# Optimization experiments

Measured on AMD Instinct MI355X. Metric: run time of the kernel, lower is better.

## Reference

```python
import jax, jax.numpy as jnp
import numpy as np

HID = 32
IN = 6
B, T = 512, 2048

def setup_inputs() -> dict:
    key = jax.random.key(0)
    ks = jax.random.split(key, 8)
    s = 1.0 / np.sqrt(HID)  # torch GRU/Linear default init scale
    return {
        "acc": jax.random.normal(ks[0], (B, T, 3), dtype=jnp.float32),
        "mag": jax.random.normal(ks[1], (B, T, 3), dtype=jnp.float32),
        "W_ih": jax.random.uniform(ks[2], (3 * HID, IN), dtype=jnp.float32, minval=-s, maxval=s),
        "W_hh": jax.random.uniform(ks[3], (3 * HID, HID), dtype=jnp.float32, minval=-s, maxval=s),
        "b_ih": jax.random.uniform(ks[4], (3 * HID,), dtype=jnp.float32, minval=-s, maxval=s),
        "b_hh": jax.random.uniform(ks[5], (3 * HID,), dtype=jnp.float32, minval=-s, maxval=s),
        "Wq": jax.random.uniform(ks[6], (4, HID), dtype=jnp.float32, minval=-s, maxval=s),
        "bq": jax.random.uniform(ks[7], (4,), dtype=jnp.float32, minval=-s, maxval=s),
    }

def _gru_seq(x, W_ih, W_hh, b_ih, b_hh):
    # x: [B,T,6] -> hidden states [B,T,HID]; PyTorch gate order: r, z, n
    gi = jnp.einsum('bti,gi->btg', x, W_ih) + b_ih  # [B,T,3H] precomputed input gates
    h0 = jnp.zeros((x.shape[0], HID), dtype=x.dtype)

    def step(h, gi_t):
        gh = h @ W_hh.T + b_hh                      # [B,3H]
        ir, iz, inn = jnp.split(gi_t, 3, axis=-1)
        hr, hz, hn = jnp.split(gh, 3, axis=-1)
        r = jax.nn.sigmoid(ir + hr)
        z = jax.nn.sigmoid(iz + hz)
        n = jnp.tanh(inn + r * hn)
        h_new = (1.0 - z) * n + z * h
        return h_new, h_new

    _, hs = jax.lax.scan(step, h0, jnp.swapaxes(gi, 0, 1))  # hs: [T,B,H]
    return jnp.swapaxes(hs, 0, 1)

def reference(acc, mag, W_ih, W_hh, b_ih, b_hh, Wq, bq):
    x = jnp.concatenate([acc, mag], axis=-1)        # [B,T,6]
    out = _gru_seq(x, W_ih, W_hh, b_ih, b_hh)       # [B,T,H]
    q = out @ Wq.T + bq                             # [B,T,4]
    return q / jnp.linalg.norm(q, axis=-1, keepdims=True)
```

## Files before the change

kernel.cpp:

```cpp
#include <hip/hip_runtime.h>
#include <hip/hip_bf16.h>

typedef float f2  __attribute__((ext_vector_type(2)));
typedef float f4v __attribute__((ext_vector_type(4)));

#ifndef __has_builtin
#define __has_builtin(x) 0
#endif

#define HID   32
#define TLEN  2048
#define BATCH 512
#define L2E   1.4426950408889634f

__device__ __forceinline__ float fast_rcp(float x) {
#if __has_builtin(__builtin_amdgcn_rcpf)
    return __builtin_amdgcn_rcpf(x);
#else
    return 1.0f / x;
#endif
}
__device__ __forceinline__ float fast_rsq(float x) {
#if __has_builtin(__builtin_amdgcn_rsqf)
    return __builtin_amdgcn_rsqf(x);
#else
    return rsqrtf(x);
#endif
}
__device__ __forceinline__ float fast_exp2(float x) {
#if __has_builtin(__builtin_amdgcn_exp2f)
    return __builtin_amdgcn_exp2f(x);
#else
    return exp2f(x);
#endif
}

__device__ __forceinline__ float xor32_sum(float x) {
#if __has_builtin(__builtin_amdgcn_permlane32_swap)
    typedef unsigned int u2v __attribute__((ext_vector_type(2)));
    u2v r = __builtin_amdgcn_permlane32_swap(__float_as_uint(x), __float_as_uint(x),
                                             false, false);
    return __uint_as_float(r.x) + __uint_as_float(r.y);
#else
    float a = x, b = x;
    asm("v_permlane32_swap_b32 %0, %1" : "+&v"(a), "+&v"(b));
    return a + b;
#endif
}

#if __has_builtin(__builtin_amdgcn_ds_swizzle)
#define SWZ_XOR(x, XORM) \
    __int_as_float(__builtin_amdgcn_ds_swizzle(__float_as_int(x), ((XORM) << 10) | 0x1F))
#else
#define SWZ_XOR(x, XORM) __shfl_xor((x), (XORM))
#endif

#define ELT(arr, i) ((i) % 4 == 0 ? (arr)[(i)/4].x : \
                     (i) % 4 == 1 ? (arr)[(i)/4].y : \
                     (i) % 4 == 2 ? (arr)[(i)/4].z : (arr)[(i)/4].w)

__global__ __launch_bounds__(64) void gru_fused_kernel(
    const float* __restrict__ acc_g, const float* __restrict__ mag_g,
    const float* __restrict__ W_ih, const float* __restrict__ W_hh,
    const float* __restrict__ b_ih, const float* __restrict__ b_hh,
    const float* __restrict__ Wq, const float* __restrict__ bq,
    float* __restrict__ out)
{
    const int lane = threadIdx.x;
    const int j    = lane & 31;
    const int half = lane >> 5;
    const int kb   = half * 16;
    const int b    = blockIdx.x;

    const int tq = lane >> 3;
    const int kq = (lane >> 2) & 1;
    const int m  = lane & 3;

    __shared__ float hbuf[8 * HID];

    f2 wr[8], wz[8], wn[8];
#pragma unroll
    for (int p = 0; p < 8; ++p) {
        wr[p] = L2E          * *reinterpret_cast<const f2*>(W_hh + (0 * HID + j) * HID + kb + 2 * p);
        wz[p] = L2E          * *reinterpret_cast<const f2*>(W_hh + (1 * HID + j) * HID + kb + 2 * p);
        wn[p] = (2.0f * L2E) * *reinterpret_cast<const f2*>(W_hh + (2 * HID + j) * HID + kb + 2 * p);
    }
    f4v wq4[4];
#pragma unroll
    for (int i = 0; i < 4; ++i)
        wq4[i] = *reinterpret_cast<const f4v*>(Wq + m * HID + kq * 16 + 4 * i);

    float wir[6], wiz[6], win[6];
#pragma unroll
    for (int i = 0; i < 6; ++i) {
        wir[i] = 0.5f * L2E * W_ih[(0 * HID + j) * 6 + i];
        wiz[i] = 0.5f * L2E * W_ih[(1 * HID + j) * 6 + i];
        win[i] = 2.0f * L2E * W_ih[(2 * HID + j) * 6 + i];
    }
    const float br_s  = 0.5f * L2E * (b_ih[0 * HID + j] + b_hh[0 * HID + j]);
    const float bz_s  = 0.5f * L2E * (b_ih[1 * HID + j] + b_hh[1 * HID + j]);
    const float bhn_s = L2E * b_hh[2 * HID + j];
    const float bin_s = 2.0f * L2E * b_ih[2 * HID + j];
    const float bqv   = bq[m];

    hbuf[7 * HID + j] = 0.0f;

    const float* accp = acc_g + (size_t)b * TLEN * 3;
    const float* magp = mag_g + (size_t)b * TLEN * 3;
    float* outp = out + (size_t)b * TLEN * 4;

    float h = 0.0f;

    auto step = [&](int sp, int ss, float a0, float a1, float a2,
                                    float m0, float m1, float m2) {
        const float* hb = &hbuf[sp * HID + kb];
        f4v A = *reinterpret_cast<const f4v*>(hb + 0);
        f4v B = *reinterpret_cast<const f4v*>(hb + 4);
        f4v C = *reinterpret_cast<const f4v*>(hb + 8);
        f4v D = *reinterpret_cast<const f4v*>(hb + 12);
        f2 hp[8] = { {A.x,A.y},{A.z,A.w},{B.x,B.y},{B.z,B.w},
                     {C.x,C.y},{C.z,C.w},{D.x,D.y},{D.z,D.w} };

        f2 dr0 = wr[0] * hp[0]; f2 dr1 = wr[4] * hp[4];
        f2 dz0 = wz[0] * hp[0]; f2 dz1 = wz[4] * hp[4];
        f2 dn0 = wn[0] * hp[0]; f2 dn1 = wn[4] * hp[4];
#pragma unroll
        for (int p = 1; p < 4; ++p) {
            dr0 += wr[p] * hp[p];  dr1 += wr[p + 4] * hp[p + 4];
            dz0 += wz[p] * hp[p];  dz1 += wz[p + 4] * hp[p + 4];
            dn0 += wn[p] * hp[p];  dn1 += wn[p + 4] * hp[p + 4];
        }

        float gr = fmaf(a2, wir[2], fmaf(a1, wir[1], fmaf(a0, wir[0], br_s)));
        gr = fmaf(m2, wir[5], fmaf(m1, wir[4], fmaf(m0, wir[3], gr)));
        float gz = fmaf(a2, wiz[2], fmaf(a1, wiz[1], fmaf(a0, wiz[0], bz_s)));
        gz = fmaf(m2, wiz[5], fmaf(m1, wiz[4], fmaf(m0, wiz[3], gz)));
        float gn = fmaf(a2, win[2], fmaf(a1, win[1], fmaf(a0, win[0], bin_s)));
        gn = fmaf(m2, win[5], fmaf(m1, win[4], fmaf(m0, win[3], gn)));

        f2 drs = dr0 + dr1; float sr = drs.x + drs.y + gr;
        f2 dzs = dz0 + dz1; float sz = dzs.x + dzs.y + gz;
        f2 dns = dn0 + dn1; float hn = dns.x + dns.y + bhn_s;
        sr = xor32_sum(sr);
        sz = xor32_sum(sz);
        hn = xor32_sum(hn);

        float r = fast_rcp(1.0f + fast_exp2(-sr));
        float z = fast_rcp(1.0f + fast_exp2(-sz));
        float ap = fmaf(r, hn, gn);
        ap = fmaxf(ap, -30.0f);
        float u  = fast_exp2(-ap);
        float nn = (1.0f - u) * fast_rcp(1.0f + u);
        h = fmaf(z, h - nn, nn);
        hbuf[ss * HID + j] = h;
    };

    auto qbatch = [&](int t0) {
        const float* hq = &hbuf[tq * HID + kq * 16];
        f4v QA = *reinterpret_cast<const f4v*>(hq + 0);
        f4v QB = *reinterpret_cast<const f4v*>(hq + 4);
        f4v QC = *reinterpret_cast<const f4v*>(hq + 8);
        f4v QD = *reinterpret_cast<const f4v*>(hq + 12);
        f4v qa = QA * wq4[0];
        qa += QB * wq4[1];
        qa += QC * wq4[2];
        qa += QD * wq4[3];
        float qp = (qa.x + qa.y) + (qa.z + qa.w);
        qp += SWZ_XOR(qp, 4);
        qp += bqv;
        float s = qp * qp;
        s += SWZ_XOR(s, 1);
        s += SWZ_XOR(s, 2);
        float qv = qp * fast_rsq(s);
        if (!(lane & 4))
            outp[(size_t)(t0 + tq) * 4 + m] = qv;
    };

    f4v xaA[6], xmA[6], xaB[6], xmB[6];
#pragma unroll
    for (int w = 0; w < 6; ++w) {
        xaA[w] = *reinterpret_cast<const f4v*>(accp + 4 * w);
        xmA[w] = *reinterpret_cast<const f4v*>(magp + 4 * w);
    }

#define WINDOW(XA, XM, XA_N, XM_N, T0)                                         \
    {                                                                          \
        const int tn = ((T0) + 8 < TLEN) ? ((T0) + 8) * 3 : 0;                 \
        _Pragma("unroll")                                                      \
        for (int w = 0; w < 6; ++w) {                                          \
            XA_N[w] = *reinterpret_cast<const f4v*>(accp + tn + 4 * w);        \
            XM_N[w] = *reinterpret_cast<const f4v*>(magp + tn + 4 * w);        \
        }                                                                      \
        _Pragma("unroll")                                                      \
        for (int s = 0; s < 8; ++s) {                                          \
            step((s + 7) & 7, s,                                               \
                 ELT(XA, 3 * s + 0), ELT(XA, 3 * s + 1), ELT(XA, 3 * s + 2),   \
                 ELT(XM, 3 * s + 0), ELT(XM, 3 * s + 1), ELT(XM, 3 * s + 2));  \
        }                                                                      \
        qbatch(T0);                                                            \
    }

    for (int t0 = 0; t0 < TLEN; t0 += 16) {
        WINDOW(xaA, xmA, xaB, xmB, t0);
        WINDOW(xaB, xmB, xaA, xmA, t0 + 8);
    }
#undef WINDOW
}

extern "C" void kernel_launch(void* const* d_in, const int* in_sizes, int n_in,
                              void* d_out, int out_size, void* d_ws, size_t ws_size,
                              hipStream_t stream) {
    const float* acc  = (const float*)d_in[0];
    const float* mag  = (const float*)d_in[1];
    const float* W_ih = (const float*)d_in[2];
    const float* W_hh = (const float*)d_in[3];
    const float* b_ih = (const float*)d_in[4];
    const float* b_hh = (const float*)d_in[5];
    const float* Wq   = (const float*)d_in[6];
    const float* bq   = (const float*)d_in[7];

    gru_fused_kernel<<<dim3(BATCH), dim3(64), 0, stream>>>(
        acc, mag, W_ih, W_hh, b_ih, b_hh, Wq, bq, (float*)d_out);
}
```

Measured before the change: 601.6 us.

## Stage input windows through shared memory with one scalar load per lane

```diff
diff --git a/kernel.cpp b/kernel.cpp
--- a/kernel.cpp
+++ b/kernel.cpp
@@ -11,6 +11,7 @@
 #define HID   32
 #define TLEN  2048
 #define BATCH 512
+#define NWIN  (TLEN / 8)
 #define L2E   1.4426950408889634f
 
 __device__ __forceinline__ float fast_rcp(float x) {
@@ -55,11 +56,7 @@
 #define SWZ_XOR(x, XORM) __shfl_xor((x), (XORM))
 #endif
 
-#define ELT(arr, i) ((i) % 4 == 0 ? (arr)[(i)/4].x : \
-                     (i) % 4 == 1 ? (arr)[(i)/4].y : \
-                     (i) % 4 == 2 ? (arr)[(i)/4].z : (arr)[(i)/4].w)
-
-__global__ __launch_bounds__(64) void gru_fused_kernel(
+__global__ __launch_bounds__(64, 1) void gru_fused_kernel(
     const float* __restrict__ acc_g, const float* __restrict__ mag_g,
     const float* __restrict__ W_ih, const float* __restrict__ W_hh,
     const float* __restrict__ b_ih, const float* __restrict__ b_hh,
@@ -68,15 +65,15 @@
 {
     const int lane = threadIdx.x;
     const int j    = lane & 31;
-    const int half = lane >> 5;
-    const int kb   = half * 16;
+    const int kb   = (lane >> 5) * 16;
     const int b    = blockIdx.x;
 
     const int tq = lane >> 3;
     const int kq = (lane >> 2) & 1;
     const int m  = lane & 3;
 
-    __shared__ float hbuf[8 * HID];
+    __shared__ __align__(16) float hbuf[8 * HID];
+    __shared__ __align__(16) float xwin[2][64];
 
     f2 wr[8], wz[8], wn[8];
 #pragma unroll
@@ -108,6 +105,16 @@
     const float* accp = acc_g + (size_t)b * TLEN * 3;
     const float* magp = mag_g + (size_t)b * TLEN * 3;
     float* outp = out + (size_t)b * TLEN * 4;
+
+    const int sW = lane >> 3, arrW = (lane >> 2) & 1, cW = lane & 3;
+    const float* xsrc = (arrW ? magp : accp) + sW * 3 + (cW < 3 ? cW : 2);
+
+    {
+        float x0 = xsrc[0];
+        float x1 = xsrc[24];
+        xwin[0][lane] = x0;
+        xwin[1][lane] = x1;
+    }
 
     float h = 0.0f;
 
@@ -176,35 +183,21 @@
             outp[(size_t)(t0 + tq) * 4 + m] = qv;
     };
 
-    f4v xaA[6], xmA[6], xaB[6], xmB[6];
-#pragma unroll
-    for (int w = 0; w < 6; ++w) {
-        xaA[w] = *reinterpret_cast<const f4v*>(accp + 4 * w);
-        xmA[w] = *reinterpret_cast<const f4v*>(magp + 4 * w);
-    }
-
-#define WINDOW(XA, XM, XA_N, XM_N, T0)                                         \
-    {                                                                          \
-        const int tn = ((T0) + 8 < TLEN) ? ((T0) + 8) * 3 : 0;                 \
-        _Pragma("unroll")                                                      \
-        for (int w = 0; w < 6; ++w) {                                          \
-            XA_N[w] = *reinterpret_cast<const f4v*>(accp + tn + 4 * w);        \
-            XM_N[w] = *reinterpret_cast<const f4v*>(magp + tn + 4 * w);        \
-        }                                                                      \
-        _Pragma("unroll")                                                      \
-        for (int s = 0; s < 8; ++s) {                                          \
-            step((s + 7) & 7, s,                                               \
-                 ELT(XA, 3 * s + 0), ELT(XA, 3 * s + 1), ELT(XA, 3 * s + 2),   \
-                 ELT(XM, 3 * s + 0), ELT(XM, 3 * s + 1), ELT(XM, 3 * s + 2));  \
-        }                                                                      \
-        qbatch(T0);                                                            \
-    }
-
-    for (int t0 = 0; t0 < TLEN; t0 += 16) {
-        WINDOW(xaA, xmA, xaB, xmB, t0);
-        WINDOW(xaB, xmB, xaA, xmA, t0 + 8);
-    }
-#undef WINDOW
+    for (int w = 0; w < NWIN; ++w) {
+        const int tn = (w + 2 < NWIN) ? (w + 2) * 24 : 0;
+        const float xstage = xsrc[tn];
+
+        const float* xw = &xwin[w & 1][0];
+#pragma unroll
+        for (int s = 0; s < 8; ++s) {
+            f4v xa = *reinterpret_cast<const f4v*>(xw + 8 * s);
+            f4v xm = *reinterpret_cast<const f4v*>(xw + 8 * s + 4);
+            step((s + 7) & 7, s, xa.x, xa.y, xa.z, xm.x, xm.y, xm.z);
+        }
+        qbatch(w * 8);
+
+        xwin[w & 1][lane] = xstage;
+    }
 }
 
 extern "C" void kernel_launch(void* const* d_in, const int* in_sizes, int n_in,
```

Result: faster. 588.9 us (-2.1%).
